# Optimization experiments

Measured on AMD Instinct MI355X. Metric: run time of the kernel, lower is better.

The kernel has to match this reference:

```python
import jax, jax.numpy as jnp
import numpy as np

K = 2  # top-k experts per token


def setup_inputs() -> dict:
    key = jax.random.key(0)
    k1, k2, k3, k4 = jax.random.split(key, 4)
    B, S, D, E, O = 4, 2048, 1024, 8, 1024
    x = jax.random.normal(k1, (B, S, D), dtype=jnp.float32)
    # gate weight: zero-init in the module; use small random values so routing is nontrivial
    Wg = jax.random.normal(k2, (E, D), dtype=jnp.float32) * 0.02
    # experts: E independent Linear(D -> O) layers, stacked
    We = jax.random.normal(k3, (E, O, D), dtype=jnp.float32) * (1.0 / np.sqrt(D))
    be = jax.random.normal(k4, (E, O), dtype=jnp.float32) * 0.01
    return {"x": x, "Wg": Wg, "We": We, "be": be}


def reference(x, Wg, We, be):
    B, S, D = x.shape
    xt = x.reshape(-1, D)                                  # [T, D]
    gate_logits = xt @ Wg.T                                # [T, E]
    vals, sel = jax.lax.top_k(gate_logits, K)              # [T, K] each
    w = jax.nn.softmax(vals.astype(jnp.float32), axis=1).astype(xt.dtype)  # [T, K]
    # all-expert outputs (E small), then gather the selected ones per token
    y = jnp.einsum('td,eod->teo', xt, We) + be[None]       # [T, E, O]
    y_sel = jnp.take_along_axis(y, sel[:, :, None], axis=1)  # [T, K, O]
    out = jnp.einsum('tk,tko->to', w, y_sel)               # [T, O]
    return out.reshape(B, S, -1)
```

## Files before the change

kernel.cpp:

```cpp
#include <hip/hip_runtime.h>
#include <hip/hip_bf16.h>

#define T_NUM 8192
#define D_DIM 1024
#define O_DIM 1024
#define E_NUM 8
#define CAP   8192
#define BM 256
#define BN 256
#define BK 64
#define NT (D_DIM / BK)

typedef float  f32x4  __attribute__((ext_vector_type(4)));
typedef __bf16 bf16x8 __attribute__((ext_vector_type(8)));

__device__ __forceinline__ void gld_lds16(const void* g, void* l) {
  __builtin_amdgcn_global_load_lds(
      (__attribute__((address_space(1))) void*)(void*)(g),
      (__attribute__((address_space(3))) void*)(l), 16, 0, 0);
}

__device__ __forceinline__ unsigned short f2bf(float f) {
  __hip_bfloat16 h = __float2bfloat16(f);
  return __builtin_bit_cast(unsigned short, h);
}

__global__ __launch_bounds__(256) void cvt_kernel(const float* __restrict__ in,
                                                  ushort* __restrict__ out, int n4) {
  int i = blockIdx.x * 256 + threadIdx.x;
  if (i >= n4) return;
  float4 v = ((const float4*)in)[i];
  ushort4 r;
  r.x = f2bf(v.x); r.y = f2bf(v.y); r.z = f2bf(v.z); r.w = f2bf(v.w);
  ((ushort4*)out)[i] = r;
}

__global__ __launch_bounds__(256) void gate_kernel(const float* __restrict__ x,
                                                   const float* __restrict__ Wg,
                                                   ushort* __restrict__ xb,
                                                   int* __restrict__ counts,
                                                   int* __restrict__ perm,
                                                   float* __restrict__ wgt_tok) {
  __shared__ int   s_sel[64][2];
  __shared__ int   s_hist[E_NUM];
  __shared__ int   s_cursor[E_NUM];

  int tid  = threadIdx.x;
  int lane = tid & 63;
  int wv   = tid >> 6;
  if (tid < E_NUM) s_hist[tid] = 0;

  int t0 = blockIdx.x * 64;

  for (int it = 0; it < 16; ++it) {
    int tl = wv * 16 + it;
    int t  = t0 + tl;
    const float4* xv = (const float4*)(x + (long)t * D_DIM);
    ushort4* xo = (ushort4*)(xb + (long)t * D_DIM);

    float acc[E_NUM];
#pragma unroll
    for (int e = 0; e < E_NUM; ++e) acc[e] = 0.f;

#pragma unroll
    for (int i = 0; i < 4; ++i) {
      float4 xf = xv[lane + i * 64];
      ushort4 r;
      r.x = f2bf(xf.x); r.y = f2bf(xf.y); r.z = f2bf(xf.z); r.w = f2bf(xf.w);
      xo[lane + i * 64] = r;
#pragma unroll
      for (int e = 0; e < E_NUM; ++e) {
        const float4* wv4 = (const float4*)(Wg + e * D_DIM);
        float4 wf = wv4[lane + i * 64];
        acc[e] += xf.x * wf.x + xf.y * wf.y + xf.z * wf.z + xf.w * wf.w;
      }
    }

    float logit[E_NUM];
#pragma unroll
    for (int e = 0; e < E_NUM; ++e) {
      float v = acc[e];
      for (int off = 32; off > 0; off >>= 1) v += __shfl_down(v, off);
      logit[e] = v;
    }

    if (lane == 0) {
      int e0 = 0; float v0 = logit[0];
#pragma unroll
      for (int e = 1; e < E_NUM; ++e)
        if (logit[e] > v0) { v0 = logit[e]; e0 = e; }
      int e1 = -1; float v1 = -1e30f;
#pragma unroll
      for (int e = 0; e < E_NUM; ++e) {
        if (e == e0) continue;
        if (logit[e] > v1) { v1 = logit[e]; e1 = e; }
      }
      float ex  = expf(v1 - v0);
      float den = 1.f + ex;
      s_sel[tl][0] = e0;
      s_sel[tl][1] = e1;
      wgt_tok[2 * t + 0] = 1.f / den;
      wgt_tok[2 * t + 1] = ex / den;
    }
  }
  __syncthreads();

  if (tid < 128) {
    int e = s_sel[tid >> 1][tid & 1];
    atomicAdd(&s_hist[e], 1);
  }
  __syncthreads();

  if (tid < E_NUM) s_cursor[tid] = atomicAdd(&counts[tid], s_hist[tid]);
  __syncthreads();

  if (tid < 128) {
    int tl = tid >> 1, k = tid & 1;
    int e  = s_sel[tl][k];
    int pos = atomicAdd(&s_cursor[e], 1);
    perm[e * CAP + pos] = ((t0 + tl) << 1) | k;
  }
}

__global__ __launch_bounds__(512, 2) void moe_gemm(const __hip_bfloat16* __restrict__ xb,
                                                   const __hip_bfloat16* __restrict__ wb,
                                                   const float* __restrict__ be,
                                                   const int* __restrict__ counts,
                                                   const int* __restrict__ perm,
                                                   ushort* __restrict__ partial) {
  int bid = blockIdx.x;
  int e  = bid >> 7;
  int rt = (bid >> 2) & 31;
  int ct = bid & 3;
  int n = counts[e];
  if (n == 0 || rt * BM >= n) return;

  __shared__ char lds[2 * 65536];

  int tid  = threadIdx.x;
  int lane = tid & 63;
  int wid  = tid >> 6;
  int wm = wid >> 2, wn = wid & 3;

  const int* permE = perm + e * CAP;

  int rbase = ((wid >> 1) << 4) + (lane & 15);
  int koff  = ((wid & 1) << 5) + ((lane >> 4) << 3);
  const __hip_bfloat16* gA[4];
  const __hip_bfloat16* gBp[4];
#pragma unroll
  for (int r = 0; r < 4; ++r) {
    int s = min(rt * BM + r * 64 + rbase, n - 1);
    gA[r]  = xb + (long)(permE[s] >> 1) * D_DIM + koff;
    gBp[r] = wb + ((long)e * O_DIM + ct * BN + r * 64 + rbase) * D_DIM + koff;
  }

  f32x4 acc[8][4];
#pragma unroll
  for (int m = 0; m < 8; ++m)
#pragma unroll
    for (int nn = 0; nn < 4; ++nn) acc[m][nn] = (f32x4){0.f, 0.f, 0.f, 0.f};

#define STAGE(buf, k0)                                                          \
  do {                                                                          \
    char* lA_ = lds + (buf) * 65536;                                            \
    char* lB_ = lds + (buf) * 65536 + 32768;                                    \
    _Pragma("unroll")                                                           \
    for (int r = 0; r < 4; ++r)                                                 \
      gld_lds16(gA[r] + (k0), lA_ + r * 8192 + wid * 1024);                     \
    _Pragma("unroll")                                                           \
    for (int r = 0; r < 4; ++r)                                                 \
      gld_lds16(gBp[r] + (k0), lB_ + r * 8192 + wid * 1024);                    \
  } while (0)

#define COMPUTE(buf)                                                            \
  do {                                                                          \
    const __hip_bfloat16* la_ = (const __hip_bfloat16*)(lds + (buf) * 65536);   \
    const __hip_bfloat16* lb_ = (const __hip_bfloat16*)(lds + (buf) * 65536 + 32768); \
    _Pragma("unroll")                                                           \
    for (int kk = 0; kk < 2; ++kk) {                                            \
      bf16x8 af[8], bfv[4];                                                     \
      _Pragma("unroll")                                                         \
      for (int m = 0; m < 8; ++m)                                               \
        af[m] = *(const bf16x8*)(la_ + ((wm * 8 + m) * 2 + kk) * 512 + lane * 8); \
      _Pragma("unroll")                                                         \
      for (int nn = 0; nn < 4; ++nn)                                            \
        bfv[nn] = *(const bf16x8*)(lb_ + ((wn * 4 + nn) * 2 + kk) * 512 + lane * 8); \
      _Pragma("unroll")                                                         \
      for (int m = 0; m < 8; ++m)                                               \
        _Pragma("unroll")                                                       \
        for (int nn = 0; nn < 4; ++nn)                                          \
          acc[m][nn] = __builtin_amdgcn_mfma_f32_16x16x32_bf16(af[m], bfv[nn],  \
                                                               acc[m][nn], 0, 0, 0); \
    }                                                                           \
  } while (0)

  STAGE(0, 0);
  __syncthreads();

  int cur = 0;
  for (int kt = 0; kt < NT - 1; ++kt) {
    STAGE(cur ^ 1, (kt + 1) * BK);
    COMPUTE(cur);
    __syncthreads();
    cur ^= 1;
  }
  COMPUTE(cur);

  int base_m = rt * BM + wm * 128;
  int base_n = ct * BN + wn * 64;
  const float* beE = be + e * O_DIM;
#pragma unroll
  for (int m = 0; m < 8; ++m) {
#pragma unroll
    for (int r = 0; r < 4; ++r) {
      int s = base_m + m * 16 + (lane >> 4) * 4 + r;
      if (s < n) {
        long entry = permE[s];
        ushort* prow = partial + entry * O_DIM;
#pragma unroll
        for (int nn = 0; nn < 4; ++nn) {
          int o = base_n + nn * 16 + (lane & 15);
          prow[o] = f2bf(acc[m][nn][r] + beE[o]);
        }
      }
    }
  }
#undef STAGE
#undef COMPUTE
}

__global__ __launch_bounds__(256) void combine_kernel(const ushort* __restrict__ partial,
                                                      const float* __restrict__ wgt_tok,
                                                      float* __restrict__ out) {
  long i = (long)blockIdx.x * 256 + threadIdx.x;
  int t = (int)(i >> 7);
  int g = (int)(i & 127);
  float w0 = wgt_tok[2 * t + 0];
  float w1 = wgt_tok[2 * t + 1];
  const uint4* p0 = (const uint4*)(partial + (long)(2 * t)     * O_DIM);
  const uint4* p1 = (const uint4*)(partial + (long)(2 * t + 1) * O_DIM);
  uint4 a = p0[g];
  uint4 b = p1[g];
  float4 o0, o1;
  uint ua[4] = {a.x, a.y, a.z, a.w};
  uint ub[4] = {b.x, b.y, b.z, b.w};
  float res[8];
#pragma unroll
  for (int j = 0; j < 4; ++j) {
    float a_lo = __builtin_bit_cast(float, ua[j] << 16);
    float a_hi = __builtin_bit_cast(float, ua[j] & 0xFFFF0000u);
    float b_lo = __builtin_bit_cast(float, ub[j] << 16);
    float b_hi = __builtin_bit_cast(float, ub[j] & 0xFFFF0000u);
    res[2 * j + 0] = w0 * a_lo + w1 * b_lo;
    res[2 * j + 1] = w0 * a_hi + w1 * b_hi;
  }
  o0 = (float4){res[0], res[1], res[2], res[3]};
  o1 = (float4){res[4], res[5], res[6], res[7]};
  float4* orow = (float4*)(out + (long)t * O_DIM + g * 8);
  orow[0] = o0;
  orow[1] = o1;
}

extern "C" void kernel_launch(void* const* d_in, const int* in_sizes, int n_in,
                              void* d_out, int out_size, void* d_ws, size_t ws_size,
                              hipStream_t stream) {
  const float* x  = (const float*)d_in[0];
  const float* Wg = (const float*)d_in[1];
  const float* We = (const float*)d_in[2];
  const float* be = (const float*)d_in[3];
  float* out = (float*)d_out;

  char* p = (char*)d_ws;
  __hip_bfloat16* xb = (__hip_bfloat16*)p;  p += (size_t)T_NUM * D_DIM * 2;
  __hip_bfloat16* wb = (__hip_bfloat16*)p;  p += (size_t)E_NUM * O_DIM * D_DIM * 2;
  int* counts = (int*)p;                    p += 256;
  int* perm   = (int*)p;                    p += (size_t)E_NUM * CAP * 4;
  float* wgt_tok = (float*)p;               p += (size_t)T_NUM * 2 * 4;
  ushort* partial = (ushort*)p;

  hipMemsetAsync(counts, 0, 256, stream);

  int n_w = E_NUM * O_DIM * D_DIM;
  cvt_kernel<<<n_w / 4 / 256, 256, 0, stream>>>(We, (ushort*)wb, n_w / 4);
  gate_kernel<<<T_NUM / 64, 256, 0, stream>>>(x, Wg, (ushort*)xb, counts, perm, wgt_tok);
  moe_gemm<<<E_NUM * 32 * 4, 512, 0, stream>>>(xb, wb, be, counts, perm, partial);
  combine_kernel<<<(T_NUM * O_DIM / 8) / 256, 256, 0, stream>>>(partial, wgt_tok, out);
}
```

Baseline: 228.8 us.

## Split MoE GEMM k-loop into eight quadrant phases with fine-grained load interleaving

Replaces the two-stage STAGE/COMPUTE loop in the expert GEMM with a schedule of eight phases per pair of K tiles. Each phase computes one quarter of the wave's output tile, issues a quarter of the next tile's global-to-LDS loads, and synchronizes with explicit vmcnt waits, raw s_barrier and s_setprio around the MFMA block. The B tile is reordered in LDS so each phase can load its half of B independently. The aim is to hide load latency and spread LDS reads across the MFMA work, at the cost of many more barriers and fragile manual waitcnt bookkeeping.

```diff
diff --git a/kernel.cpp b/kernel.cpp
--- a/kernel.cpp
+++ b/kernel.cpp
@@ -41,9 +41,9 @@
                                                    int* __restrict__ counts,
                                                    int* __restrict__ perm,
                                                    float* __restrict__ wgt_tok) {
-  __shared__ int   s_sel[64][2];
-  __shared__ int   s_hist[E_NUM];
-  __shared__ int   s_cursor[E_NUM];
+  __shared__ int s_sel[64][2];
+  __shared__ int s_hist[E_NUM];
+  __shared__ int s_cursor[E_NUM];
 
   int tid  = threadIdx.x;
   int lane = tid & 63;
@@ -144,16 +144,24 @@
 
   const int* permE = perm + e * CAP;
 
-  int rbase = ((wid >> 1) << 4) + (lane & 15);
-  int koff  = ((wid & 1) << 5) + ((lane >> 4) << 3);
+  int arow_in = (wid >> 1) * 16 + (lane & 15);
+  int akoff   = ((wid & 1) << 5) + ((lane >> 4) << 3);
   const __hip_bfloat16* gA[4];
-  const __hip_bfloat16* gBp[4];
 #pragma unroll
   for (int r = 0; r < 4; ++r) {
-    int s = min(rt * BM + r * 64 + rbase, n - 1);
-    gA[r]  = xb + (long)(permE[s] >> 1) * D_DIM + koff;
-    gBp[r] = wb + ((long)e * O_DIM + ct * BN + r * 64 + rbase) * D_DIM + koff;
-  }
+    int s = min(rt * BM + r * 64 + arow_in, n - 1);
+    gA[r] = xb + (long)(permE[s] >> 1) * D_DIM + akoff;
+  }
+
+  const __hip_bfloat16* gB[4];
+#pragma unroll
+  for (int nh = 0; nh < 2; ++nh)
+#pragma unroll
+    for (int p = 0; p < 2; ++p) {
+      int nn = (p * 2 + (wid >> 2)) * 4 + nh * 2 + ((wid >> 1) & 1);
+      gB[nh * 2 + p] = wb + ((long)e * O_DIM + ct * BN + nn * 16 + (lane & 15)) * D_DIM
+                       + ((wid & 1) << 5) + ((lane >> 4) << 3);
+    }
 
   f32x4 acc[8][4];
 #pragma unroll
@@ -161,51 +169,76 @@
 #pragma unroll
     for (int nn = 0; nn < 4; ++nn) acc[m][nn] = (f32x4){0.f, 0.f, 0.f, 0.f};
 
-#define STAGE(buf, k0)                                                          \
-  do {                                                                          \
-    char* lA_ = lds + (buf) * 65536;                                            \
-    char* lB_ = lds + (buf) * 65536 + 32768;                                    \
-    _Pragma("unroll")                                                           \
-    for (int r = 0; r < 4; ++r)                                                 \
-      gld_lds16(gA[r] + (k0), lA_ + r * 8192 + wid * 1024);                     \
-    _Pragma("unroll")                                                           \
-    for (int r = 0; r < 4; ++r)                                                 \
-      gld_lds16(gBp[r] + (k0), lB_ + r * 8192 + wid * 1024);                    \
+#define SA(buf, r, k0)  gld_lds16(gA[r] + (k0), lds + (buf) * 65536 + (r) * 8192 + wid * 1024)
+#define SB(buf, nh, p, k0) gld_lds16(gB[(nh) * 2 + (p)] + (k0), \
+    lds + (buf) * 65536 + 32768 + ((nh) * 16 + (p) * 8 + wid) * 1024)
+#define STAGE_AH(buf, mh, k0) do { SA(buf, (mh), k0); SA(buf, (mh) + 2, k0); } while (0)
+#define STAGE_BH(buf, nh, k0) do { SB(buf, (nh), 0, k0); SB(buf, (nh), 1, k0); } while (0)
+#define VMCNT4 asm volatile("s_waitcnt vmcnt(4)" ::: "memory")
+#define VMCNT0 asm volatile("s_waitcnt vmcnt(0)" ::: "memory")
+#define NOPST  ((void)0)
+
+#define PHASE(buf, mh, nh, WCNT, ...)                                            \
+  do {                                                                           \
+    const __hip_bfloat16* la_ = (const __hip_bfloat16*)(lds + (buf) * 65536);    \
+    const __hip_bfloat16* lb_ = (const __hip_bfloat16*)(lds + (buf) * 65536 + 32768); \
+    bf16x8 af[4][2], bv[2][2];                                                   \
+    _Pragma("unroll")                                                            \
+    for (int i = 0; i < 4; ++i)                                                  \
+      _Pragma("unroll")                                                          \
+      for (int kk = 0; kk < 2; ++kk)                                             \
+        af[i][kk] = *(const bf16x8*)(la_ + ((wm * 8 + (mh) * 4 + i) * 2 + kk) * 512 + lane * 8); \
+    _Pragma("unroll")                                                            \
+    for (int nl = 0; nl < 2; ++nl)                                               \
+      _Pragma("unroll")                                                          \
+      for (int kk = 0; kk < 2; ++kk)                                             \
+        bv[nl][kk] = *(const bf16x8*)(lb_ + ((nh) * 16 + wn * 4 + nl * 2 + kk) * 512 + lane * 8); \
+    __VA_ARGS__;                                                                 \
+    WCNT;                                                                        \
+    __builtin_amdgcn_s_barrier();                                                \
+    __builtin_amdgcn_s_setprio(1);                                               \
+    _Pragma("unroll")                                                            \
+    for (int i = 0; i < 4; ++i)                                                  \
+      _Pragma("unroll")                                                          \
+      for (int nl = 0; nl < 2; ++nl)                                             \
+        _Pragma("unroll")                                                        \
+        for (int kk = 0; kk < 2; ++kk)                                           \
+          acc[(mh) * 4 + i][(nh) * 2 + nl] = __builtin_amdgcn_mfma_f32_16x16x32_bf16( \
+              af[i][kk], bv[nl][kk], acc[(mh) * 4 + i][(nh) * 2 + nl], 0, 0, 0); \
+    __builtin_amdgcn_s_setprio(0);                                               \
+    __builtin_amdgcn_s_barrier();                                                \
   } while (0)
 
-#define COMPUTE(buf)                                                            \
-  do {                                                                          \
-    const __hip_bfloat16* la_ = (const __hip_bfloat16*)(lds + (buf) * 65536);   \
-    const __hip_bfloat16* lb_ = (const __hip_bfloat16*)(lds + (buf) * 65536 + 32768); \
-    _Pragma("unroll")                                                           \
-    for (int kk = 0; kk < 2; ++kk) {                                            \
-      bf16x8 af[8], bfv[4];                                                     \
-      _Pragma("unroll")                                                         \
-      for (int m = 0; m < 8; ++m)                                               \
-        af[m] = *(const bf16x8*)(la_ + ((wm * 8 + m) * 2 + kk) * 512 + lane * 8); \
-      _Pragma("unroll")                                                         \
-      for (int nn = 0; nn < 4; ++nn)                                            \
-        bfv[nn] = *(const bf16x8*)(lb_ + ((wn * 4 + nn) * 2 + kk) * 512 + lane * 8); \
-      _Pragma("unroll")                                                         \
-      for (int m = 0; m < 8; ++m)                                               \
-        _Pragma("unroll")                                                       \
-        for (int nn = 0; nn < 4; ++nn)                                          \
-          acc[m][nn] = __builtin_amdgcn_mfma_f32_16x16x32_bf16(af[m], bfv[nn],  \
-                                                               acc[m][nn], 0, 0, 0); \
-    }                                                                           \
-  } while (0)
-
-  STAGE(0, 0);
-  __syncthreads();
-
-  int cur = 0;
-  for (int kt = 0; kt < NT - 1; ++kt) {
-    STAGE(cur ^ 1, (kt + 1) * BK);
-    COMPUTE(cur);
-    __syncthreads();
-    cur ^= 1;
-  }
-  COMPUTE(cur);
+  STAGE_AH(0, 0, 0);  STAGE_BH(0, 0, 0);
+  STAGE_AH(0, 1, 0);  STAGE_BH(0, 1, 0);
+  STAGE_AH(1, 0, BK); STAGE_BH(1, 0, BK);
+  VMCNT4;
+  __builtin_amdgcn_s_barrier();
+
+  for (int j = 0; j < 7; ++j) {
+    int kA = (2 * j + 1) * BK;
+    int kB = (2 * j + 2) * BK;
+    int kC = (2 * j + 3) * BK;
+    PHASE(0, 0, 0, NOPST,  STAGE_AH(1, 1, kA));
+    PHASE(0, 0, 1, NOPST,  STAGE_BH(1, 1, kA));
+    PHASE(0, 1, 0, NOPST,  STAGE_AH(0, 0, kB));
+    PHASE(0, 1, 1, VMCNT4, STAGE_BH(0, 0, kB));
+    PHASE(1, 0, 0, NOPST,  STAGE_AH(0, 1, kB));
+    PHASE(1, 0, 1, NOPST,  STAGE_BH(0, 1, kB));
+    PHASE(1, 1, 0, NOPST,  STAGE_AH(1, 0, kC));
+    PHASE(1, 1, 1, VMCNT4, STAGE_BH(1, 0, kC));
+  }
+  {
+    int kA = 15 * BK;
+    PHASE(0, 0, 0, NOPST,  STAGE_AH(1, 1, kA));
+    PHASE(0, 0, 1, NOPST,  STAGE_BH(1, 1, kA));
+    PHASE(0, 1, 0, NOPST,  NOPST);
+    PHASE(0, 1, 1, VMCNT0, NOPST);
+    PHASE(1, 0, 0, NOPST,  NOPST);
+    PHASE(1, 0, 1, NOPST,  NOPST);
+    PHASE(1, 1, 0, NOPST,  NOPST);
+    PHASE(1, 1, 1, NOPST,  NOPST);
+  }
 
   int base_m = rt * BM + wm * 128;
   int base_n = ct * BN + wn * 64;
@@ -226,8 +259,11 @@
       }
     }
   }
-#undef STAGE
-#undef COMPUTE
+#undef SA
+#undef SB
+#undef STAGE_AH
+#undef STAGE_BH
+#undef PHASE
 }
 
 __global__ __launch_bounds__(256) void combine_kernel(const ushort* __restrict__ partial,
@@ -242,7 +278,6 @@
   const uint4* p1 = (const uint4*)(partial + (long)(2 * t + 1) * O_DIM);
   uint4 a = p0[g];
   uint4 b = p1[g];
-  float4 o0, o1;
   uint ua[4] = {a.x, a.y, a.z, a.w};
   uint ub[4] = {b.x, b.y, b.z, b.w};
   float res[8];
@@ -255,11 +290,9 @@
     res[2 * j + 0] = w0 * a_lo + w1 * b_lo;
     res[2 * j + 1] = w0 * a_hi + w1 * b_hi;
   }
-  o0 = (float4){res[0], res[1], res[2], res[3]};
-  o1 = (float4){res[4], res[5], res[6], res[7]};
   float4* orow = (float4*)(out + (long)t * O_DIM + g * 8);
-  orow[0] = o0;
-  orow[1] = o1;
+  orow[0] = (float4){res[0], res[1], res[2], res[3]};
+  orow[1] = (float4){res[4], res[5], res[6], res[7]};
 }
 
 extern "C" void kernel_launch(void* const* d_in, const int* in_sizes, int n_in,
```

After: 221.2 us. 3.3% less time.
